# Optimization experiments

Hardware: AMD Instinct MI355X
Metric: run time of the kernel (lower is better)

Reference implementation:

```python
import jax, jax.numpy as jnp
import numpy as np

# DCNv2 config (matches init_kwargs)
CHI, CHO = 64, 64
K = 3; KK = K * K
G = 1                 # deformable_groups
S, P, D = 1, 1, 1     # stride, padding, dilation
B, H, W = 4, 128, 256


def setup_inputs() -> dict:
    key = jax.random.key(0)
    k1, k2, k3, k4 = jax.random.split(key, 4)
    x = jax.random.normal(k1, (B, CHI, H, W), jnp.float32)
    # offset/mask conv params (small init so sampled offsets stay modest, like trained nets)
    w_off = jax.random.normal(k2, (3 * G * KK, CHI, K, K), jnp.float32) * 0.01
    b_off = jax.random.normal(k3, (3 * G * KK,), jnp.float32) * 0.01
    # main deformable conv weight (kaiming-like scale) and zero bias
    weight = jax.random.normal(k4, (CHO, CHI, K, K), jnp.float32) * (1.0 / np.sqrt(CHI * KK))
    bias = jnp.zeros((CHO,), jnp.float32)
    return {"x": x, "w_off": w_off, "b_off": b_off, "weight": weight, "bias": bias}


def _deform_conv(x, w_off, b_off, weight, bias):
    Bq, C, Hh, Ww = x.shape
    # offset/mask conv: [B, 3*G*KK, Ho, Wo]
    om = jax.lax.conv_general_dilated(
        x, w_off, (S, S), ((P, P), (P, P)),
        dimension_numbers=("NCHW", "OIHW", "NCHW")) + b_off[None, :, None, None]
    Ho, Wo = om.shape[2], om.shape[3]
    # torchvision layout: offset[:, 2*(g*KK+k)+{0:y,1:x}]
    off = om[:, : 2 * G * KK].reshape(Bq, G, KK, 2, Ho, Wo)
    mask = jax.nn.sigmoid(om[:, 2 * G * KK :]).reshape(Bq, G, KK, Ho, Wo)

    kk = jnp.arange(KK)
    ky = (kk // K).astype(jnp.float32)
    kx = (kk % K).astype(jnp.float32)
    base_y = jnp.arange(Ho, dtype=jnp.float32)[None, :, None] * S - P + ky[:, None, None] * D  # [KK,Ho,1]
    base_x = jnp.arange(Wo, dtype=jnp.float32)[None, None, :] * S - P + kx[:, None, None] * D  # [KK,1,Wo]
    sy = base_y[None, None] + off[:, :, :, 0]  # [B,G,KK,Ho,Wo] absolute sample y
    sx = base_x[None, None] + off[:, :, :, 1]

    y0 = jnp.floor(sy); x0 = jnp.floor(sx)
    dy = sy - y0; dx = sx - x0
    y0i = y0.astype(jnp.int32); x0i = x0.astype(jnp.int32)

    Cg = C // G
    xf = x.reshape(Bq, G, Cg, Hh * Ww)
    gather = jax.vmap(jax.vmap(lambda xg, idx: xg[:, idx]))  # -> [B,G,Cg,KK,Ho,Wo]

    def corner(iy, ix, w):
        valid = (iy >= 0) & (iy < Hh) & (ix >= 0) & (ix < Ww)
        idx = jnp.clip(iy, 0, Hh - 1) * Ww + jnp.clip(ix, 0, Ww - 1)
        return gather(xf, idx) * jnp.where(valid, w, 0.0)[:, :, None]

    # bilinear sample with zero padding (out-of-bounds corners contribute 0)
    sampled = (corner(y0i,     x0i,     (1 - dy) * (1 - dx))
             + corner(y0i,     x0i + 1, (1 - dy) * dx)
             + corner(y0i + 1, x0i,     dy * (1 - dx))
             + corner(y0i + 1, x0i + 1, dy * dx))
    sampled = sampled * mask[:, :, None]  # modulation

    wr = weight.reshape(CHO, G, Cg, KK)
    out = jnp.einsum("bgckhw,ogck->bohw", sampled, wr) + bias[None, :, None, None]
    return out


def reference(x, w_off, b_off, weight, bias):
    return _deform_conv(x, w_off, b_off, weight, bias)
```

## Files before the change

### kernel.cpp

```cpp
#include <hip/hip_runtime.h>
#include <math.h>

#define CHI 64
#define CHO 64
#define BB 4
#define HH 128
#define WW 256
#define HWSZ (HH * WW)
#define NSTEP 18
#define WROWS 9
#define WCOLS 23
#define WSTRIDE 144
#define WENTRIES (WROWS * WCOLS)

typedef float f32x4 __attribute__((ext_vector_type(4)));
typedef _Float16 f16x8 __attribute__((ext_vector_type(8)));

__device__ __attribute__((aligned(16))) ushort g_xT[BB * HWSZ * CHI];
__device__ __attribute__((aligned(16))) ushort g_wB2[NSTEP * 4 * 64 * 8];
__device__ __attribute__((aligned(16))) ushort g_wOffB2[NSTEP * 2 * 64 * 8];

__device__ __forceinline__ ushort f2h(float f) {
    _Float16 h = (_Float16)f;
    return __builtin_bit_cast(ushort, h);
}
__device__ __forceinline__ uint32_t pkh2(float a, float b) {
    return (uint32_t)f2h(a) | ((uint32_t)f2h(b) << 16);
}
__device__ __forceinline__ _Float16 hlo(uint32_t u) {
    return __builtin_bit_cast(_Float16, (ushort)(u & 0xffffu));
}
__device__ __forceinline__ _Float16 hhi(uint32_t u) {
    return __builtin_bit_cast(_Float16, (ushort)(u >> 16));
}

__global__ void prep(const float* __restrict__ weight, const float* __restrict__ w_off) {
    int idx = blockIdx.x * 256 + threadIdx.x;
    if (idx < NSTEP * 4 * 64 * 8) {
        int e = idx & 7, t = idx >> 3;
        int l = t & 63; t >>= 6;
        int n = t & 3, s = t >> 2;
        int o = n * 16 + (l & 15);
        int K = s * 32 + (l >> 4) * 8 + e;
        int kh = K >> 6, c = K & 63;
        g_wB2[idx] = f2h(weight[(o * CHI + c) * 9 + kh]);
    }
    if (idx < NSTEP * 2 * 64 * 8) {
        int e = idx & 7, t = idx >> 3;
        int l = t & 63; t >>= 6;
        int j = t & 1, s = t >> 1;
        int o = j * 16 + (l & 15);
        int K = s * 32 + (l >> 4) * 8 + e;
        int kh = K >> 6, c = K & 63;
        g_wOffB2[idx] = (o < 27) ? f2h(w_off[(o * CHI + c) * 9 + kh]) : (ushort)0;
    }
}

__global__ __launch_bounds__(256) void transform(const float* __restrict__ x) {
    __shared__ ushort t[64][68];
    const int tid = threadIdx.x;
    const int wv = tid >> 6, lane = tid & 63;
    const int pb = blockIdx.x * 64;
    const int b = pb >> 15;
    const int pin = pb & (HWSZ - 1);
    const float* __restrict__ xb = x + (size_t)b * CHI * HWSZ + pin;
#pragma unroll
    for (int i = 0; i < 16; ++i) {
        const int c = wv * 16 + i;
        t[lane][c] = f2h(xb[(size_t)c * HWSZ + lane]);
    }
    __syncthreads();
    const int px = tid >> 2, cb = (tid & 3) * 16;
    const uint32_t* __restrict__ row = (const uint32_t*)&t[px][cb];
    uint4 v0, v1;
    v0.x = row[0]; v0.y = row[1]; v0.z = row[2]; v0.w = row[3];
    v1.x = row[4]; v1.y = row[5]; v1.z = row[6]; v1.w = row[7];
    uint4* __restrict__ dst = (uint4*)&g_xT[(size_t)(pb + px) * CHI + cb];
    dst[0] = v0; dst[1] = v1;
}

union U8 { uint32_t u[4]; f16x8 v; };

__global__ __launch_bounds__(256, 2) void dcn_win(
    const float* __restrict__ b_off, const float* __restrict__ bias,
    float* __restrict__ out)
{
    __shared__ __align__(16) char win[WENTRIES * WSTRIDE];
    __shared__ union {
        float om[4][16][33];
        struct {
            uint2 pw[4][16][9];
            uint  yx[4][16][9];
        } p;
    } sh;

    const int tid = threadIdx.x;
    const int wv = tid >> 6, l = tid & 63;
    const int lr = l & 15, lg = l >> 4;
    const int blk = blockIdx.x;
    const int b = blk >> 9;
    const int t512 = blk & 511;
    const int hb = (t512 >> 4) * 4;
    const int wb = (t512 & 15) * 16;
    const char* __restrict__ xtb = (const char*)g_xT + (size_t)b * HWSZ * (CHI * 2);
    const int lgo = lg * 16;

    for (int i = tid; i < WENTRIES * 8; i += 256) {
        const int e = i >> 3, q = i & 7;
        const int r = e / WCOLS;
        const int j = e - r * WCOLS;
        const int gy = min(max(hb - 2 + r, 0), HH - 1);
        const int gx = min(max(wb - 3 + j, 0), WW - 1);
        const uint4 v = *(const uint4*)(xtb + ((size_t)(gy * WW + gx)) * (CHI * 2) + q * 16);
        *(uint4*)(win + e * WSTRIDE + q * 16) = v;
    }

    f16x8 bA[12], bB[12];
#define LOADB(BUF, G)                                                        \
    _Pragma("unroll")                                                        \
    for (int i = 0; i < 12; ++i)                                             \
        BUF[i] = *(const f16x8*)&g_wOffB2[((size_t)((G) * 12 + i) * 64 + l) * 8];

    LOADB(bA, 0)
    __syncthreads();

    {
        const int h = hb + wv;
        const int w = wb + lr;
        f32x4 acc0 = {0.f, 0.f, 0.f, 0.f}, acc1 = {0.f, 0.f, 0.f, 0.f};

#define COMPUTE6(BUF, G)                                                     \
    _Pragma("unroll")                                                        \
    for (int ss = 0; ss < 6; ++ss) {                                         \
        const int s = (G) * 6 + ss;                                          \
        const int kh = s >> 1, ky = kh / 3, kx = kh % 3;                     \
        const bool vld = ((unsigned)(h + ky - 1) < HH) & ((unsigned)(w + kx - 1) < WW); \
        const int e = (wv + ky + 1) * WCOLS + (lr + kx + 2);                 \
        U8 Av;                                                               \
        Av.v = *(const f16x8*)(win + e * WSTRIDE + (s & 1) * 64 + lgo);      \
        if (!vld) { Av.u[0] = 0; Av.u[1] = 0; Av.u[2] = 0; Av.u[3] = 0; }    \
        acc0 = __builtin_amdgcn_mfma_f32_16x16x32_f16(Av.v, BUF[ss * 2 + 0], acc0, 0, 0, 0); \
        acc1 = __builtin_amdgcn_mfma_f32_16x16x32_f16(Av.v, BUF[ss * 2 + 1], acc1, 0, 0, 0); \
    }

        LOADB(bB, 1)
        COMPUTE6(bA, 0)
        LOADB(bA, 2)
        COMPUTE6(bB, 1)
        COMPUTE6(bA, 2)

#pragma unroll
        for (int i = 0; i < 4; ++i) {
            sh.om[wv][lg * 4 + i][lr]      = acc0[i];
            sh.om[wv][lg * 4 + i][16 + lr] = acc1[i];
        }
    }
#undef COMPUTE6
#undef LOADB
    __syncthreads();

    f16x8 wfc[8], wfn[8];
#pragma unroll
    for (int n = 0; n < 8; ++n)
        wfc[n] = *(const f16x8*)&g_wB2[((size_t)(0 * 8 + n) * 64 + l) * 8];
#pragma unroll
    for (int n = 0; n < 8; ++n)
        wfn[n] = *(const f16x8*)&g_wB2[((size_t)(1 * 8 + n) * 64 + l) * 8];

    float vyr[3], vxr[3], vmr[3];
#pragma unroll
    for (int t = 0; t < 3; ++t) {
        const int kh = lg + t * 4;
        if (kh < 9) {
            vyr[t] = sh.om[wv][lr][2 * kh];
            vxr[t] = sh.om[wv][lr][2 * kh + 1];
            vmr[t] = sh.om[wv][lr][18 + kh];
        }
    }
    __syncthreads();
#pragma unroll
    for (int t = 0; t < 3; ++t) {
        const int kh = lg + t * 4;
        if (kh < 9) {
            const int h2 = hb + wv;
            const int w2 = wb + lr;
            float offy = vyr[t] + b_off[2 * kh];
            float offx = vxr[t] + b_off[2 * kh + 1];
            float mm   = vmr[t] + b_off[18 + kh];
            mm = 1.f / (1.f + __expf(-mm));
            const float sy = (float)(h2 - 1 + kh / 3) + offy;
            const float sx = (float)(w2 - 1 + kh % 3) + offx;
            const float fy = floorf(sy), fx = floorf(sx);
            const int y0 = (int)fy, x0 = (int)fx;
            const float dy = sy - fy, dx = sx - fx;
            const float wy0 = (1.f - dy) * mm, wy1 = dy * mm;
            float w00 = wy0 * (1.f - dx), w01 = wy0 * dx;
            float w10 = wy1 * (1.f - dx), w11 = wy1 * dx;
            const bool vy0 = (unsigned)y0 < HH, vy1 = (unsigned)(y0 + 1) < HH;
            const bool vx0 = (unsigned)x0 < WW, vx1 = (unsigned)(x0 + 1) < WW;
            if (!(vy0 & vx0)) w00 = 0.f;
            if (!(vy0 & vx1)) w01 = 0.f;
            if (!(vy1 & vx0)) w10 = 0.f;
            if (!(vy1 & vx1)) w11 = 0.f;
            sh.p.pw[wv][lr][kh] = make_uint2(pkh2(w00, w01), pkh2(w10, w11));
            sh.p.yx[wv][lr][kh] = (uint32_t)(uint16_t)(int16_t)y0 |
                                  ((uint32_t)(uint16_t)(int16_t)x0 << 16);
        }
    }
    __syncthreads();

    f32x4 acc[4];
#pragma unroll
    for (int n = 0; n < 4; ++n) acc[n] = (f32x4){0.f, 0.f, 0.f, 0.f};

    const char* __restrict__ xh0 = xtb + lgo;
    const char* __restrict__ xh1 = xtb + 64 + lgo;

    f16x8 cc[8];
    uint2 pwc;

#define GATHER(DST, YX)                                                      \
    {                                                                        \
        const int y0 = (int)(short)((YX) & 0xffffu);                         \
        const int x0 = (int)(short)((YX) >> 16);                             \
        const int cy0 = min(max(y0, 0), HH - 1), cy1 = min(max(y0 + 1, 0), HH - 1); \
        const int cx0 = min(max(x0, 0), WW - 1), cx1 = min(max(x0 + 1, 0), WW - 1); \
        const int r0 = cy0 - hb + 2, r1 = cy1 - hb + 2;                      \
        const int j0 = cx0 - wb + 3, j1 = cx1 - wb + 3;                      \
        const bool okw = ((unsigned)r0 < WROWS) & ((unsigned)r1 < WROWS) &   \
                         ((unsigned)j0 < WCOLS) & ((unsigned)j1 < WCOLS);    \
        if (__all(okw)) {                                                    \
            const int l00 = (r0 * WCOLS + j0) * WSTRIDE;                     \
            const int l01 = (r0 * WCOLS + j1) * WSTRIDE;                     \
            const int l10 = (r1 * WCOLS + j0) * WSTRIDE;                     \
            const int l11 = (r1 * WCOLS + j1) * WSTRIDE;                     \
            DST[0] = *(const f16x8*)(win + l00 + lgo);                       \
            DST[1] = *(const f16x8*)(win + l01 + lgo);                       \
            DST[2] = *(const f16x8*)(win + l10 + lgo);                       \
            DST[3] = *(const f16x8*)(win + l11 + lgo);                       \
            DST[4] = *(const f16x8*)(win + l00 + lgo + 64);                  \
            DST[5] = *(const f16x8*)(win + l01 + lgo + 64);                  \
            DST[6] = *(const f16x8*)(win + l10 + lgo + 64);                  \
            DST[7] = *(const f16x8*)(win + l11 + lgo + 64);                  \
        } else {                                                             \
            const int o00 = (cy0 * WW + cx0) * (CHI * 2);                    \
            const int o01 = (cy0 * WW + cx1) * (CHI * 2);                    \
            const int o10 = (cy1 * WW + cx0) * (CHI * 2);                    \
            const int o11 = (cy1 * WW + cx1) * (CHI * 2);                    \
            DST[0] = *(const f16x8*)(xh0 + o00);                             \
            DST[1] = *(const f16x8*)(xh0 + o01);                             \
            DST[2] = *(const f16x8*)(xh0 + o10);                             \
            DST[3] = *(const f16x8*)(xh0 + o11);                             \
            DST[4] = *(const f16x8*)(xh1 + o00);                             \
            DST[5] = *(const f16x8*)(xh1 + o01);                             \
            DST[6] = *(const f16x8*)(xh1 + o10);                             \
            DST[7] = *(const f16x8*)(xh1 + o11);                             \
        }                                                                    \
    }

    {
        const uint32_t yx0 = sh.p.yx[wv][lr][0];
        pwc = sh.p.pw[wv][lr][0];
        GATHER(cc, yx0)
    }

#pragma unroll 3
    for (int kh = 0; kh < 9; ++kh) {
        f16x8 wfn2[8], cn[8];
        uint2 pw_n; uint32_t yx_n;
        if (kh < 7) {
#pragma unroll
            for (int n = 0; n < 8; ++n)
                wfn2[n] = *(const f16x8*)&g_wB2[((size_t)((kh + 2) * 8 + n) * 64 + l) * 8];
        }
        if (kh < 8) {
            yx_n = sh.p.yx[wv][lr][kh + 1];
            pw_n = sh.p.pw[wv][lr][kh + 1];
            GATHER(cn, yx_n)
        }
        const _Float16 w00 = hlo(pwc.x), w01 = hhi(pwc.x);
        const _Float16 w10 = hlo(pwc.y), w11 = hhi(pwc.y);
        const f16x8 W00 = {w00, w00, w00, w00, w00, w00, w00, w00};
        const f16x8 W01 = {w01, w01, w01, w01, w01, w01, w01, w01};
        const f16x8 W10 = {w10, w10, w10, w10, w10, w10, w10, w10};
        const f16x8 W11 = {w11, w11, w11, w11, w11, w11, w11, w11};

        const f16x8 A0 = cc[0] * W00 + cc[1] * W01 + cc[2] * W10 + cc[3] * W11;
        const f16x8 A1 = cc[4] * W00 + cc[5] * W01 + cc[6] * W10 + cc[7] * W11;

#pragma unroll
        for (int n = 0; n < 4; ++n)
            acc[n] = __builtin_amdgcn_mfma_f32_16x16x32_f16(A0, wfc[n], acc[n], 0, 0, 0);
#pragma unroll
        for (int n = 0; n < 4; ++n)
            acc[n] = __builtin_amdgcn_mfma_f32_16x16x32_f16(A1, wfc[4 + n], acc[n], 0, 0, 0);

        if (kh < 8) {
            pwc = pw_n;
#pragma unroll
            for (int n = 0; n < 8; ++n) { cc[n] = cn[n]; wfc[n] = wfn[n]; }
            if (kh < 7) {
#pragma unroll
                for (int n = 0; n < 8; ++n) wfn[n] = wfn2[n];
            }
        }
    }
#undef GATHER

#pragma unroll
    for (int n = 0; n < 4; ++n) {
        const int o = n * 16 + lr;
        const float bo = bias[o];
        float* op = out + (((size_t)b * CHO + o) * HH + hb + wv) * WW + wb + lg * 4;
        f32x4 r;
#pragma unroll
        for (int i = 0; i < 4; ++i) r[i] = acc[n][i] + bo;
        *(f32x4*)op = r;
    }
}

extern "C" void kernel_launch(void* const* d_in, const int* in_sizes, int n_in,
                              void* d_out, int out_size, void* d_ws, size_t ws_size,
                              hipStream_t stream) {
    const float* x      = (const float*)d_in[0];
    const float* w_off  = (const float*)d_in[1];
    const float* b_off  = (const float*)d_in[2];
    const float* weight = (const float*)d_in[3];
    const float* bias   = (const float*)d_in[4];
    float* out = (float*)d_out;

    prep<<<144, 256, 0, stream>>>(weight, w_off);
    transform<<<2048, 256, 0, stream>>>(x);
    dcn_win<<<2048, 256, 0, stream>>>(b_off, bias, out);
}
```

Measured before the change: 68.58 us.

## Fuse NCHW-to-NHWC fp16 transform into deformable conv window load

New measurement: 79.52 us. +15.9%, slower.

```diff
diff --git a/kernel.cpp b/kernel.cpp
--- a/kernel.cpp
+++ b/kernel.cpp
@@ -16,7 +16,6 @@
 typedef float f32x4 __attribute__((ext_vector_type(4)));
 typedef _Float16 f16x8 __attribute__((ext_vector_type(8)));
 
-__device__ __attribute__((aligned(16))) ushort g_xT[BB * HWSZ * CHI];
 __device__ __attribute__((aligned(16))) ushort g_wB2[NSTEP * 4 * 64 * 8];
 __device__ __attribute__((aligned(16))) ushort g_wOffB2[NSTEP * 2 * 64 * 8];
 
@@ -56,34 +55,11 @@
     }
 }
 
-__global__ __launch_bounds__(256) void transform(const float* __restrict__ x) {
-    __shared__ ushort t[64][68];
-    const int tid = threadIdx.x;
-    const int wv = tid >> 6, lane = tid & 63;
-    const int pb = blockIdx.x * 64;
-    const int b = pb >> 15;
-    const int pin = pb & (HWSZ - 1);
-    const float* __restrict__ xb = x + (size_t)b * CHI * HWSZ + pin;
-#pragma unroll
-    for (int i = 0; i < 16; ++i) {
-        const int c = wv * 16 + i;
-        t[lane][c] = f2h(xb[(size_t)c * HWSZ + lane]);
-    }
-    __syncthreads();
-    const int px = tid >> 2, cb = (tid & 3) * 16;
-    const uint32_t* __restrict__ row = (const uint32_t*)&t[px][cb];
-    uint4 v0, v1;
-    v0.x = row[0]; v0.y = row[1]; v0.z = row[2]; v0.w = row[3];
-    v1.x = row[4]; v1.y = row[5]; v1.z = row[6]; v1.w = row[7];
-    uint4* __restrict__ dst = (uint4*)&g_xT[(size_t)(pb + px) * CHI + cb];
-    dst[0] = v0; dst[1] = v1;
-}
-
 union U8 { uint32_t u[4]; f16x8 v; };
 
 __global__ __launch_bounds__(256, 2) void dcn_win(
-    const float* __restrict__ b_off, const float* __restrict__ bias,
-    float* __restrict__ out)
+    const float* __restrict__ x, const float* __restrict__ b_off,
+    const float* __restrict__ bias, float* __restrict__ out)
 {
     __shared__ __align__(16) char win[WENTRIES * WSTRIDE];
     __shared__ union {
@@ -102,17 +78,20 @@
     const int t512 = blk & 511;
     const int hb = (t512 >> 4) * 4;
     const int wb = (t512 & 15) * 16;
-    const char* __restrict__ xtb = (const char*)g_xT + (size_t)b * HWSZ * (CHI * 2);
+    const float* __restrict__ xw = x + (size_t)b * CHI * HWSZ;
     const int lgo = lg * 16;
 
-    for (int i = tid; i < WENTRIES * 8; i += 256) {
-        const int e = i >> 3, q = i & 7;
+    for (int i = tid; i < 32 * WENTRIES; i += 256) {
+        const int cp = i / WENTRIES;
+        const int e = i - cp * WENTRIES;
         const int r = e / WCOLS;
         const int j = e - r * WCOLS;
         const int gy = min(max(hb - 2 + r, 0), HH - 1);
         const int gx = min(max(wb - 3 + j, 0), WW - 1);
-        const uint4 v = *(const uint4*)(xtb + ((size_t)(gy * WW + gx)) * (CHI * 2) + q * 16);
-        *(uint4*)(win + e * WSTRIDE + q * 16) = v;
+        const size_t gi = (size_t)gy * WW + gx;
+        const float v0 = xw[(size_t)(2 * cp) * HWSZ + gi];
+        const float v1 = xw[(size_t)(2 * cp + 1) * HWSZ + gi];
+        *(uint32_t*)(win + e * WSTRIDE + cp * 4) = pkh2(v0, v1);
     }
 
     f16x8 bA[12], bB[12];
@@ -213,11 +192,18 @@
 #pragma unroll
     for (int n = 0; n < 4; ++n) acc[n] = (f32x4){0.f, 0.f, 0.f, 0.f};
 
-    const char* __restrict__ xh0 = xtb + lgo;
-    const char* __restrict__ xh1 = xtb + 64 + lgo;
-
     f16x8 cc[8];
     uint2 pwc;
+
+#define FBLOAD(DST, GI, CB)                                                  \
+    {                                                                        \
+        U8 t_;                                                               \
+        _Pragma("unroll")                                                    \
+        for (int q = 0; q < 4; ++q)                                          \
+            t_.u[q] = pkh2(xw[(size_t)((CB) + 2 * q) * HWSZ + (GI)],         \
+                           xw[(size_t)((CB) + 2 * q + 1) * HWSZ + (GI)]);    \
+        DST = t_.v;                                                          \
+    }
 
 #define GATHER(DST, YX)                                                      \
     {                                                                        \
@@ -243,18 +229,19 @@
             DST[6] = *(const f16x8*)(win + l10 + lgo + 64);                  \
             DST[7] = *(const f16x8*)(win + l11 + lgo + 64);                  \
         } else {                                                             \
-            const int o00 = (cy0 * WW + cx0) * (CHI * 2);                    \
-            const int o01 = (cy0 * WW + cx1) * (CHI * 2);                    \
-            const int o10 = (cy1 * WW + cx0) * (CHI * 2);                    \
-            const int o11 = (cy1 * WW + cx1) * (CHI * 2);                    \
-            DST[0] = *(const f16x8*)(xh0 + o00);                             \
-            DST[1] = *(const f16x8*)(xh0 + o01);                             \
-            DST[2] = *(const f16x8*)(xh0 + o10);                             \
-            DST[3] = *(const f16x8*)(xh0 + o11);                             \
-            DST[4] = *(const f16x8*)(xh1 + o00);                             \
-            DST[5] = *(const f16x8*)(xh1 + o01);                             \
-            DST[6] = *(const f16x8*)(xh1 + o10);                             \
-            DST[7] = *(const f16x8*)(xh1 + o11);                             \
+            const size_t g00 = (size_t)cy0 * WW + cx0;                       \
+            const size_t g01 = (size_t)cy0 * WW + cx1;                       \
+            const size_t g10 = (size_t)cy1 * WW + cx0;                       \
+            const size_t g11 = (size_t)cy1 * WW + cx1;                       \
+            const int cb0 = lg * 8, cb1 = 32 + lg * 8;                       \
+            FBLOAD(DST[0], g00, cb0)                                         \
+            FBLOAD(DST[1], g01, cb0)                                         \
+            FBLOAD(DST[2], g10, cb0)                                         \
+            FBLOAD(DST[3], g11, cb0)                                         \
+            FBLOAD(DST[4], g00, cb1)                                         \
+            FBLOAD(DST[5], g01, cb1)                                         \
+            FBLOAD(DST[6], g10, cb1)                                         \
+            FBLOAD(DST[7], g11, cb1)                                         \
         }                                                                    \
     }
 
@@ -306,6 +293,7 @@
         }
     }
 #undef GATHER
+#undef FBLOAD
 
 #pragma unroll
     for (int n = 0; n < 4; ++n) {
@@ -330,6 +318,5 @@
     float* out = (float*)d_out;
 
     prep<<<144, 256, 0, stream>>>(weight, w_off);
-    transform<<<2048, 256, 0, stream>>>(x);
-    dcn_win<<<2048, 256, 0, stream>>>(b_off, bias, out);
-}
+    dcn_win<<<2048, 256, 0, stream>>>(x, b_off, bias, out);
+}
```
